# Kernel optimization log

Measured on AMD Instinct MI355X. Metric: run time of the kernel, lower is better.

The kernel has to match this reference:

```python
import jax, jax.numpy as jnp
import numpy as np

KERNEL_SIZE = 11
SIGMA = 1.5
DATA_RANGE = 1.0
C1 = (0.01 * DATA_RANGE) ** 2
C2 = (0.03 * DATA_RANGE) ** 2


def _gaussian_kernel_2d(kernel_size=KERNEL_SIZE, sigma=SIGMA):
    coords = jnp.arange(kernel_size, dtype=jnp.float32) - kernel_size // 2
    g1d = jnp.exp(-coords ** 2 / (2.0 * sigma ** 2))
    g2d = g1d[:, None] * g1d[None, :]
    return g2d / g2d.sum()  # [K, K]


def _depthwise_blur(x, kernel2d):
    # x: [B, C, H, W]; kernel2d: [K, K] -> depthwise conv, SAME padding
    C = x.shape[1]
    k = jnp.broadcast_to(kernel2d[None, None], (C, 1, KERNEL_SIZE, KERNEL_SIZE)).astype(x.dtype)
    pad = KERNEL_SIZE // 2
    return jax.lax.conv_general_dilated(
        x, k,
        window_strides=(1, 1),
        padding=((pad, pad), (pad, pad)),
        dimension_numbers=('NCHW', 'OIHW', 'NCHW'),
        feature_group_count=C,
    )


def reference(pred, target):
    kernel2d = _gaussian_kernel_2d()
    mu_p = _depthwise_blur(pred, kernel2d)
    mu_t = _depthwise_blur(target, kernel2d)
    mu_p_sq = mu_p * mu_p
    mu_t_sq = mu_t * mu_t
    mu_pt = mu_p * mu_t
    sigma_p_sq = _depthwise_blur(pred * pred, kernel2d) - mu_p_sq
    sigma_t_sq = _depthwise_blur(target * target, kernel2d) - mu_t_sq
    sigma_pt = _depthwise_blur(pred * target, kernel2d) - mu_pt
    sigma_p_sq = jnp.clip(sigma_p_sq, 0.0, None)
    sigma_t_sq = jnp.clip(sigma_t_sq, 0.0, None)
    numerator = (2.0 * mu_pt + C1) * (2.0 * sigma_pt + C2)
    denominator = (mu_p_sq + mu_t_sq + C1) * (sigma_p_sq + sigma_t_sq + C2)
    ssim_map = numerator / denominator
    return 1.0 - jnp.mean(ssim_map)


def setup_inputs() -> dict:
    key = jax.random.key(0)
    k1, k2 = jax.random.split(key)
    shape = (16, 3, 512, 512)
    pred = jax.random.uniform(k1, shape, dtype=jnp.float32)
    target = jax.random.uniform(k2, shape, dtype=jnp.float32)
    return {"pred": pred, "target": target}
```

## Files before the change

kernel.cpp:

```cpp
#include <hip/hip_runtime.h>
#include <hip/hip_fp16.h>


#define WIDTH  512
#define HEIGHT 512
#define TW 64
#define SH 128
#define RING 48
#define RST 56
#define TILES_X 8
#define TILES_Y (HEIGHT / SH)
#define PLANES 48
#define NBLK (TILES_X * TILES_Y * PLANES)
#define NPIXF 12582912.0f

typedef _Float16 half8_t __attribute__((ext_vector_type(8)));
typedef float f32x4_t __attribute__((ext_vector_type(4)));
typedef unsigned int u32x4_t __attribute__((ext_vector_type(4)));

__device__ __forceinline__ float wsel(int i) {
    unsigned a = (unsigned)i;
    float r = 0.f;
    if (a == 5u)              r = 0.26601168f;
    if (a == 4u || a == 6u)   r = 0.21300566f;
    if (a == 3u || a == 7u)   r = 0.10936069f;
    if (a == 2u || a == 8u)   r = 0.03600077f;
    if (a == 1u || a == 9u)   r = 0.00759881f;
    if (a == 0u || a == 10u)  r = 0.00102839f;
    return r;
}

__global__ __launch_bounds__(256, 4)
void ssim_main(const float* __restrict__ pred,
               const float* __restrict__ tgt,
               float* __restrict__ partial) {
    __shared__ __align__(16) __half s_ring[4][TW][RST];
    __shared__ __align__(16) __half s_pl[4][16][80];
    __shared__ float s_red[4];

    const int tid  = threadIdx.x;
    const int wv   = tid >> 6;
    const int lane = tid & 63;
    const int r15  = lane & 15;
    const int g4   = lane >> 4;
    const int x0 = blockIdx.x * TW;
    const int y0 = blockIdx.y * SH;
    const size_t plane_off = (size_t)blockIdx.z * (WIDTH * HEIGHT);
    const float* P = pred + plane_off;
    const float* T = tgt + plane_off;
    const bool x_int = (x0 >= 8) && (x0 + TW + 8 <= WIDTH);

    const float s1 = 2.f * ((float)(_Float16)0.00102839f + (float)(_Float16)0.00759881f
                   + (float)(_Float16)0.03600077f + (float)(_Float16)0.10936069f
                   + (float)(_Float16)0.21300566f) + (float)(_Float16)0.26601168f;
    const float a   = s1 * s1;
    const float C1A = a * a * 1e-4f;
    const float C2A = a * a * 9e-4f;

    half8_t Bh, Bv;
#pragma unroll
    for (int jj = 0; jj < 8; ++jj) {
        int k = g4 * 8 + jj;
        Bv[jj] = (_Float16)wsel(k - r15);
        Bh[jj] = (_Float16)wsel(k - r15 - 3);
    }

    const int  erow0 = tid >> 4, ecq0 = tid & 15;
    const bool e2    = tid < 64;
    const int  erow1 = tid >> 2, ecq1 = 16 + (tid & 3);

    auto ldquad = [&](int gybase, int row, int cq, float4& p, float4& t) {
        int gy = gybase + row;
        if (gy < 0) gy = 0;
        if (gy > HEIGHT - 1) gy = HEIGHT - 1;
        int gx = x0 - 8 + cq * 4;
        if (gx < 0) gx = 0;
        if (gx > WIDTH - 4) gx = WIDTH - 4;
        const size_t ro = (size_t)gy << 9;
        p = *(const float4*)(P + ro + gx);
        t = *(const float4*)(T + ro + gx);
    };
    auto load_gen = [&](int gybase, float4& p0, float4& t0,
                        float4& p1, float4& t1) {
        ldquad(gybase, erow0, ecq0, p0, t0);
        if (e2) ldquad(gybase, erow1, ecq1, p1, t1);
    };

    auto equad = [&](int gybase, int row, int cq, float4 pv, float4 tv) {
        int gy = gybase + row;
        if ((unsigned)gy >= (unsigned)HEIGHT) {
            pv.x = pv.y = pv.z = pv.w = 0.f;
            tv.x = tv.y = tv.z = tv.w = 0.f;
        } else if (!x_int) {
            int gx0 = x0 - 8 + cq * 4;
            if ((unsigned)(gx0 + 0) >= (unsigned)WIDTH) { pv.x = 0.f; tv.x = 0.f; }
            if ((unsigned)(gx0 + 1) >= (unsigned)WIDTH) { pv.y = 0.f; tv.y = 0.f; }
            if ((unsigned)(gx0 + 2) >= (unsigned)WIDTH) { pv.z = 0.f; tv.z = 0.f; }
            if ((unsigned)(gx0 + 3) >= (unsigned)WIDTH) { pv.w = 0.f; tv.w = 0.f; }
        }
        float u0 = fmaf(pv.x, pv.x, tv.x * tv.x), v0 = pv.x * tv.x;
        float u1 = fmaf(pv.y, pv.y, tv.y * tv.y), v1 = pv.y * tv.y;
        float u2 = fmaf(pv.z, pv.z, tv.z * tv.z), v2 = pv.z * tv.z;
        float u3 = fmaf(pv.w, pv.w, tv.w * tv.w), v3 = pv.w * tv.w;
        uint2 wp, wt, wu, wvv;
        wp.x  = __builtin_bit_cast(unsigned, __floats2half2_rn(pv.x, pv.y));
        wp.y  = __builtin_bit_cast(unsigned, __floats2half2_rn(pv.z, pv.w));
        wt.x  = __builtin_bit_cast(unsigned, __floats2half2_rn(tv.x, tv.y));
        wt.y  = __builtin_bit_cast(unsigned, __floats2half2_rn(tv.z, tv.w));
        wu.x  = __builtin_bit_cast(unsigned, __floats2half2_rn(u0, u1));
        wu.y  = __builtin_bit_cast(unsigned, __floats2half2_rn(u2, u3));
        wvv.x = __builtin_bit_cast(unsigned, __floats2half2_rn(v0, v1));
        wvv.y = __builtin_bit_cast(unsigned, __floats2half2_rn(v2, v3));
        *(uint2*)&s_pl[0][row][cq * 4] = wp;
        *(uint2*)&s_pl[1][row][cq * 4] = wt;
        *(uint2*)&s_pl[2][row][cq * 4] = wu;
        *(uint2*)&s_pl[3][row][cq * 4] = wvv;
    };
    auto ewise = [&](int gybase, float4 p0, float4 t0, float4 p1, float4 t1) {
        equad(gybase, erow0, ecq0, p0, t0);
        if (e2) equad(gybase, erow1, ecq1, p1, t1);
    };

    auto hblur = [&](int relbase) {
        int s0 = relbase + 4 * g4;
        if (s0 >= 96) s0 -= 96; else if (s0 >= 48) s0 -= 48;
        const int colA = (wv << 4) + r15;
        const int acol = (wv << 4) + (g4 << 3);
#pragma unroll
        for (int q = 0; q < 4; ++q) {
            u32x4_t ra = *(const u32x4_t*)&s_pl[q][r15][acol];
            f32x4_t z = {0.f, 0.f, 0.f, 0.f};
            f32x4_t d = __builtin_amdgcn_mfma_f32_16x16x32_f16(
                __builtin_bit_cast(half8_t, ra), Bh, z, 0, 0, 0);
            uint2 pk;
            pk.x = __builtin_bit_cast(unsigned, __floats2half2_rn(d[0], d[1]));
            pk.y = __builtin_bit_cast(unsigned, __floats2half2_rn(d[2], d[3]));
            *(uint2*)&s_ring[q][colA][s0] = pk;
        }
    };

    float lsum = 0.f;

    auto vblur = [&](int jstep) {
        int sg = 16 * jstep + (g4 << 3);
        if (sg >= 96) sg -= 96; else if (sg >= 48) sg -= 48;
        const int colA = (wv << 4) + r15;
        f32x4_t acc[4];
#pragma unroll
        for (int q = 0; q < 4; ++q) {
            u32x4_t ra = *(const u32x4_t*)&s_ring[q][colA][sg];
            f32x4_t z = {0.f, 0.f, 0.f, 0.f};
            acc[q] = __builtin_amdgcn_mfma_f32_16x16x32_f16(
                __builtin_bit_cast(half8_t, ra), Bv, z, 0, 0, 0);
        }
#pragma unroll
        for (int r = 0; r < 4; ++r) {
            float mp = acc[0][r], mt = acc[1][r];
            float U  = acc[2][r], V  = acc[3][r];
            float mpt  = mp * mt;
            float B2   = fmaf(mp, mp, mt * mt);
            float S    = fmaf(a, V, -mpt);
            float Ssum = fmaf(a, U, -B2);
            float num = fmaf(2.f, mpt, C1A) * fmaf(2.f, S, C2A);
            float den = (B2 + C1A) * (Ssum + C2A);
            lsum += __fdividef(num, den);
        }
    };

    float4 ap0, at0, ap1, at1;
    float4 bp0, bt0, bp1, bt1;
    load_gen(y0 - 5, ap0, at0, ap1, at1);
    load_gen(y0 + 7, bp0, bt0, bp1, bt1);
    {
        u32x4_t z4 = {0u, 0u, 0u, 0u};
#pragma unroll
        for (int i = 0; i < 7; ++i)
            ((u32x4_t*)s_ring)[tid + 256 * i] = z4;
    }
    ewise(y0 - 5, ap0, at0, ap1, at1);
    __syncthreads();
    hblur(0);
    load_gen(y0 + 23, ap0, at0, ap1, at1);
    __syncthreads();
    ewise(y0 + 7, bp0, bt0, bp1, bt1);
    __syncthreads();
    hblur(12);
    __syncthreads();

#pragma unroll 1
    for (int j = 0; j < 8; ++j) {
        if (j < 7) ewise(y0 + 16 * j + 23, ap0, at0, ap1, at1);
        __syncthreads();
        if (j < 6) load_gen(y0 + 16 * (j + 1) + 23, ap0, at0, ap1, at1);
        if (j < 7) hblur(16 * j + 28);
        vblur(j);
        __syncthreads();
    }

#pragma unroll
    for (int off = 32; off > 0; off >>= 1) lsum += __shfl_down(lsum, off);
    if ((tid & 63) == 0) s_red[tid >> 6] = lsum;
    __syncthreads();
    if (tid == 0) {
        partial[(blockIdx.z * TILES_Y + blockIdx.y) * TILES_X + blockIdx.x] =
            s_red[0] + s_red[1] + s_red[2] + s_red[3];
    }
}

__global__ __launch_bounds__(256)
void ssim_final(const float* __restrict__ partial, float* __restrict__ out) {
    __shared__ float s_red[4];
    float s = 0.f;
    for (int i = threadIdx.x; i < NBLK; i += 256) s += partial[i];
#pragma unroll
    for (int off = 32; off > 0; off >>= 1) s += __shfl_down(s, off);
    if ((threadIdx.x & 63) == 0) s_red[threadIdx.x >> 6] = s;
    __syncthreads();
    if (threadIdx.x == 0) {
        float total = s_red[0] + s_red[1] + s_red[2] + s_red[3];
        out[0] = 1.0f - total / NPIXF;
    }
}

extern "C" void kernel_launch(void* const* d_in, const int* in_sizes, int n_in,
                              void* d_out, int out_size, void* d_ws, size_t ws_size,
                              hipStream_t stream) {
    const float* pred = (const float*)d_in[0];
    const float* tgt  = (const float*)d_in[1];
    float* partial = (float*)d_ws;

    dim3 grid(TILES_X, TILES_Y, PLANES);
    ssim_main<<<grid, dim3(256), 0, stream>>>(pred, tgt, partial);
    ssim_final<<<1, dim3(256), 0, stream>>>(partial, (float*)d_out);
}
```

Measured before the change: 130.6 us.

## Build horizontal-blur MFMA fragments directly from global loads, drop staging LDS

```diff
diff --git a/kernel.cpp b/kernel.cpp
--- a/kernel.cpp
+++ b/kernel.cpp
@@ -30,12 +30,15 @@
     return r;
 }
 
+__device__ __forceinline__ unsigned cvt2(float a, float b) {
+    return __builtin_bit_cast(unsigned, __floats2half2_rn(a, b));
+}
+
 __global__ __launch_bounds__(256, 4)
 void ssim_main(const float* __restrict__ pred,
                const float* __restrict__ tgt,
                float* __restrict__ partial) {
     __shared__ __align__(16) __half s_ring[4][TW][RST];
-    __shared__ __align__(16) __half s_pl[4][16][80];
     __shared__ float s_red[4];
 
     const int tid  = threadIdx.x;
@@ -48,7 +51,9 @@
     const size_t plane_off = (size_t)blockIdx.z * (WIDTH * HEIGHT);
     const float* P = pred + plane_off;
     const float* T = tgt + plane_off;
-    const bool x_int = (x0 >= 8) && (x0 + TW + 8 <= WIDTH);
+
+    const int gxb  = x0 - 8 + (wv << 4) + (g4 << 3);
+    const int colA = (wv << 4) + r15;
 
     const float s1 = 2.f * ((float)(_Float16)0.00102839f + (float)(_Float16)0.00759881f
                    + (float)(_Float16)0.03600077f + (float)(_Float16)0.10936069f
@@ -65,78 +70,67 @@
         Bh[jj] = (_Float16)wsel(k - r15 - 3);
     }
 
-    const int  erow0 = tid >> 4, ecq0 = tid & 15;
-    const bool e2    = tid < 64;
-    const int  erow1 = tid >> 2, ecq1 = 16 + (tid & 3);
-
-    auto ldquad = [&](int gybase, int row, int cq, float4& p, float4& t) {
-        int gy = gybase + row;
+    auto load8 = [&](int gybase, float4& p0, float4& p1,
+                     float4& t0, float4& t1) {
+        int gy = gybase + r15;
         if (gy < 0) gy = 0;
         if (gy > HEIGHT - 1) gy = HEIGHT - 1;
-        int gx = x0 - 8 + cq * 4;
-        if (gx < 0) gx = 0;
-        if (gx > WIDTH - 4) gx = WIDTH - 4;
-        const size_t ro = (size_t)gy << 9;
-        p = *(const float4*)(P + ro + gx);
-        t = *(const float4*)(T + ro + gx);
-    };
-    auto load_gen = [&](int gybase, float4& p0, float4& t0,
-                        float4& p1, float4& t1) {
-        ldquad(gybase, erow0, ecq0, p0, t0);
-        if (e2) ldquad(gybase, erow1, ecq1, p1, t1);
-    };
-
-    auto equad = [&](int gybase, int row, int cq, float4 pv, float4 tv) {
-        int gy = gybase + row;
-        if ((unsigned)gy >= (unsigned)HEIGHT) {
-            pv.x = pv.y = pv.z = pv.w = 0.f;
-            tv.x = tv.y = tv.z = tv.w = 0.f;
-        } else if (!x_int) {
-            int gx0 = x0 - 8 + cq * 4;
-            if ((unsigned)(gx0 + 0) >= (unsigned)WIDTH) { pv.x = 0.f; tv.x = 0.f; }
-            if ((unsigned)(gx0 + 1) >= (unsigned)WIDTH) { pv.y = 0.f; tv.y = 0.f; }
-            if ((unsigned)(gx0 + 2) >= (unsigned)WIDTH) { pv.z = 0.f; tv.z = 0.f; }
-            if ((unsigned)(gx0 + 3) >= (unsigned)WIDTH) { pv.w = 0.f; tv.w = 0.f; }
-        }
-        float u0 = fmaf(pv.x, pv.x, tv.x * tv.x), v0 = pv.x * tv.x;
-        float u1 = fmaf(pv.y, pv.y, tv.y * tv.y), v1 = pv.y * tv.y;
-        float u2 = fmaf(pv.z, pv.z, tv.z * tv.z), v2 = pv.z * tv.z;
-        float u3 = fmaf(pv.w, pv.w, tv.w * tv.w), v3 = pv.w * tv.w;
-        uint2 wp, wt, wu, wvv;
-        wp.x  = __builtin_bit_cast(unsigned, __floats2half2_rn(pv.x, pv.y));
-        wp.y  = __builtin_bit_cast(unsigned, __floats2half2_rn(pv.z, pv.w));
-        wt.x  = __builtin_bit_cast(unsigned, __floats2half2_rn(tv.x, tv.y));
-        wt.y  = __builtin_bit_cast(unsigned, __floats2half2_rn(tv.z, tv.w));
-        wu.x  = __builtin_bit_cast(unsigned, __floats2half2_rn(u0, u1));
-        wu.y  = __builtin_bit_cast(unsigned, __floats2half2_rn(u2, u3));
-        wvv.x = __builtin_bit_cast(unsigned, __floats2half2_rn(v0, v1));
-        wvv.y = __builtin_bit_cast(unsigned, __floats2half2_rn(v2, v3));
-        *(uint2*)&s_pl[0][row][cq * 4] = wp;
-        *(uint2*)&s_pl[1][row][cq * 4] = wt;
-        *(uint2*)&s_pl[2][row][cq * 4] = wu;
-        *(uint2*)&s_pl[3][row][cq * 4] = wvv;
-    };
-    auto ewise = [&](int gybase, float4 p0, float4 t0, float4 p1, float4 t1) {
-        equad(gybase, erow0, ecq0, p0, t0);
-        if (e2) equad(gybase, erow1, ecq1, p1, t1);
-    };
-
-    auto hblur = [&](int relbase) {
+        int gxc = gxb;
+        if (gxc < 0) gxc = 0;
+        if (gxc > WIDTH - 8) gxc = WIDTH - 8;
+        const float* pr = P + ((size_t)gy << 9) + gxc;
+        const float* tr = T + ((size_t)gy << 9) + gxc;
+        p0 = *(const float4*)pr; p1 = *(const float4*)(pr + 4);
+        t0 = *(const float4*)tr; t1 = *(const float4*)(tr + 4);
+    };
+
+    auto make_frags = [&](int gybase, float4 pv0, float4 pv1,
+                          float4 tv0, float4 tv1, u32x4_t* F) {
+        int gy = gybase + r15;
+        const bool ok = ((unsigned)gy < (unsigned)HEIGHT) &&
+                        ((unsigned)gxb <= (unsigned)(WIDTH - 8));
+        if (!ok) {
+            pv0.x = pv0.y = pv0.z = pv0.w = 0.f;
+            pv1.x = pv1.y = pv1.z = pv1.w = 0.f;
+            tv0.x = tv0.y = tv0.z = tv0.w = 0.f;
+            tv1.x = tv1.y = tv1.z = tv1.w = 0.f;
+        }
+        float u0 = fmaf(pv0.x, pv0.x, tv0.x * tv0.x), v0 = pv0.x * tv0.x;
+        float u1 = fmaf(pv0.y, pv0.y, tv0.y * tv0.y), v1 = pv0.y * tv0.y;
+        float u2 = fmaf(pv0.z, pv0.z, tv0.z * tv0.z), v2 = pv0.z * tv0.z;
+        float u3 = fmaf(pv0.w, pv0.w, tv0.w * tv0.w), v3 = pv0.w * tv0.w;
+        float u4 = fmaf(pv1.x, pv1.x, tv1.x * tv1.x), v4 = pv1.x * tv1.x;
+        float u5 = fmaf(pv1.y, pv1.y, tv1.y * tv1.y), v5 = pv1.y * tv1.y;
+        float u6 = fmaf(pv1.z, pv1.z, tv1.z * tv1.z), v6 = pv1.z * tv1.z;
+        float u7 = fmaf(pv1.w, pv1.w, tv1.w * tv1.w), v7 = pv1.w * tv1.w;
+        u32x4_t Pu, Tu, Uu, Vu;
+        Pu[0] = cvt2(pv0.x, pv0.y); Pu[1] = cvt2(pv0.z, pv0.w);
+        Pu[2] = cvt2(pv1.x, pv1.y); Pu[3] = cvt2(pv1.z, pv1.w);
+        Tu[0] = cvt2(tv0.x, tv0.y); Tu[1] = cvt2(tv0.z, tv0.w);
+        Tu[2] = cvt2(tv1.x, tv1.y); Tu[3] = cvt2(tv1.z, tv1.w);
+        Uu[0] = cvt2(u0, u1); Uu[1] = cvt2(u2, u3);
+        Uu[2] = cvt2(u4, u5); Uu[3] = cvt2(u6, u7);
+        Vu[0] = cvt2(v0, v1); Vu[1] = cvt2(v2, v3);
+        Vu[2] = cvt2(v4, v5); Vu[3] = cvt2(v6, v7);
+        F[0] = Pu; F[1] = Tu; F[2] = Uu; F[3] = Vu;
+    };
+
+    auto hcompute = [&](const u32x4_t* F, uint2* dpk) {
+#pragma unroll
+        for (int q = 0; q < 4; ++q) {
+            f32x4_t z = {0.f, 0.f, 0.f, 0.f};
+            f32x4_t d = __builtin_amdgcn_mfma_f32_16x16x32_f16(
+                __builtin_bit_cast(half8_t, F[q]), Bh, z, 0, 0, 0);
+            dpk[q].x = cvt2(d[0], d[1]);
+            dpk[q].y = cvt2(d[2], d[3]);
+        }
+    };
+    auto hstore = [&](const uint2* dpk, int relbase) {
         int s0 = relbase + 4 * g4;
         if (s0 >= 96) s0 -= 96; else if (s0 >= 48) s0 -= 48;
-        const int colA = (wv << 4) + r15;
-        const int acol = (wv << 4) + (g4 << 3);
-#pragma unroll
-        for (int q = 0; q < 4; ++q) {
-            u32x4_t ra = *(const u32x4_t*)&s_pl[q][r15][acol];
-            f32x4_t z = {0.f, 0.f, 0.f, 0.f};
-            f32x4_t d = __builtin_amdgcn_mfma_f32_16x16x32_f16(
-                __builtin_bit_cast(half8_t, ra), Bh, z, 0, 0, 0);
-            uint2 pk;
-            pk.x = __builtin_bit_cast(unsigned, __floats2half2_rn(d[0], d[1]));
-            pk.y = __builtin_bit_cast(unsigned, __floats2half2_rn(d[2], d[3]));
-            *(uint2*)&s_ring[q][colA][s0] = pk;
-        }
+#pragma unroll
+        for (int q = 0; q < 4; ++q)
+            *(uint2*)&s_ring[q][colA][s0] = dpk[q];
     };
 
     float lsum = 0.f;
@@ -144,7 +138,6 @@
     auto vblur = [&](int jstep) {
         int sg = 16 * jstep + (g4 << 3);
         if (sg >= 96) sg -= 96; else if (sg >= 48) sg -= 48;
-        const int colA = (wv << 4) + r15;
         f32x4_t acc[4];
 #pragma unroll
         for (int q = 0; q < 4; ++q) {
@@ -167,33 +160,41 @@
         }
     };
 
-    float4 ap0, at0, ap1, at1;
-    float4 bp0, bt0, bp1, bt1;
-    load_gen(y0 - 5, ap0, at0, ap1, at1);
-    load_gen(y0 + 7, bp0, bt0, bp1, bt1);
+    float4 rp0, rp1, rt0, rt1;
+    float4 sp0, sp1, st0, st1;
+    load8(y0 - 5, rp0, rp1, rt0, rt1);
+    load8(y0 + 7, sp0, sp1, st0, st1);
     {
         u32x4_t z4 = {0u, 0u, 0u, 0u};
 #pragma unroll
         for (int i = 0; i < 7; ++i)
             ((u32x4_t*)s_ring)[tid + 256 * i] = z4;
     }
-    ewise(y0 - 5, ap0, at0, ap1, at1);
-    __syncthreads();
-    hblur(0);
-    load_gen(y0 + 23, ap0, at0, ap1, at1);
-    __syncthreads();
-    ewise(y0 + 7, bp0, bt0, bp1, bt1);
-    __syncthreads();
-    hblur(12);
+    u32x4_t F2[4], F1[4];
+    uint2 d2[4], d1[4];
+    make_frags(y0 - 5, rp0, rp1, rt0, rt1, F2);
+    hcompute(F2, d2);
+    make_frags(y0 + 7, sp0, sp1, st0, st1, F1);
+    hcompute(F1, d1);
+    load8(y0 + 23, rp0, rp1, rt0, rt1);
+    __syncthreads();
+    hstore(d2, 0);
+    __syncthreads();
+    hstore(d1, 12);
     __syncthreads();
 
 #pragma unroll 1
     for (int j = 0; j < 8; ++j) {
-        if (j < 7) ewise(y0 + 16 * j + 23, ap0, at0, ap1, at1);
+        u32x4_t F[4];
+        uint2 dpk[4];
+        if (j < 7) {
+            make_frags(y0 + 16 * j + 23, rp0, rp1, rt0, rt1, F);
+            hcompute(F, dpk);
+        }
+        vblur(j);
         __syncthreads();
-        if (j < 6) load_gen(y0 + 16 * (j + 1) + 23, ap0, at0, ap1, at1);
-        if (j < 7) hblur(16 * j + 28);
-        vblur(j);
+        if (j < 7) hstore(dpk, 16 * j + 28);
+        if (j < 6) load8(y0 + 16 * (j + 1) + 23, rp0, rp1, rt0, rt1);
         __syncthreads();
     }
 
```

After: 137.2 us. +5.0%, slower.

## Double-buffer global prefetch and reblock ring LDS layout to avoid bank conflicts

Applied to the files above, without the earlier changes.

```diff
diff --git a/kernel.cpp b/kernel.cpp
--- a/kernel.cpp
+++ b/kernel.cpp
@@ -7,7 +7,6 @@
 #define TW 64
 #define SH 128
 #define RING 48
-#define RST 56
 #define TILES_X 8
 #define TILES_Y (HEIGHT / SH)
 #define PLANES 48
@@ -30,12 +29,16 @@
     return r;
 }
 
+__device__ __forceinline__ unsigned cvt2(float a, float b) {
+    return __builtin_bit_cast(unsigned, __floats2half2_rn(a, b));
+}
+
 __global__ __launch_bounds__(256, 4)
 void ssim_main(const float* __restrict__ pred,
                const float* __restrict__ tgt,
                float* __restrict__ partial) {
-    __shared__ __align__(16) __half s_ring[4][TW][RST];
-    __shared__ __align__(16) __half s_pl[4][16][80];
+    __shared__ __align__(16) __half s_ring[4][RING / 8][TW][8];
+    __shared__ __align__(16) __half s_pl[4][16][88];
     __shared__ float s_red[4];
 
     const int tid  = threadIdx.x;
@@ -50,6 +53,8 @@
     const float* T = tgt + plane_off;
     const bool x_int = (x0 >= 8) && (x0 + TW + 8 <= WIDTH);
 
+    const int colA = (wv << 4) + r15;
+
     const float s1 = 2.f * ((float)(_Float16)0.00102839f + (float)(_Float16)0.00759881f
                    + (float)(_Float16)0.03600077f + (float)(_Float16)0.10936069f
                    + (float)(_Float16)0.21300566f) + (float)(_Float16)0.26601168f;
@@ -103,14 +108,10 @@
         float u2 = fmaf(pv.z, pv.z, tv.z * tv.z), v2 = pv.z * tv.z;
         float u3 = fmaf(pv.w, pv.w, tv.w * tv.w), v3 = pv.w * tv.w;
         uint2 wp, wt, wu, wvv;
-        wp.x  = __builtin_bit_cast(unsigned, __floats2half2_rn(pv.x, pv.y));
-        wp.y  = __builtin_bit_cast(unsigned, __floats2half2_rn(pv.z, pv.w));
-        wt.x  = __builtin_bit_cast(unsigned, __floats2half2_rn(tv.x, tv.y));
-        wt.y  = __builtin_bit_cast(unsigned, __floats2half2_rn(tv.z, tv.w));
-        wu.x  = __builtin_bit_cast(unsigned, __floats2half2_rn(u0, u1));
-        wu.y  = __builtin_bit_cast(unsigned, __floats2half2_rn(u2, u3));
-        wvv.x = __builtin_bit_cast(unsigned, __floats2half2_rn(v0, v1));
-        wvv.y = __builtin_bit_cast(unsigned, __floats2half2_rn(v2, v3));
+        wp.x  = cvt2(pv.x, pv.y); wp.y  = cvt2(pv.z, pv.w);
+        wt.x  = cvt2(tv.x, tv.y); wt.y  = cvt2(tv.z, tv.w);
+        wu.x  = cvt2(u0, u1);     wu.y  = cvt2(u2, u3);
+        wvv.x = cvt2(v0, v1);     wvv.y = cvt2(v2, v3);
         *(uint2*)&s_pl[0][row][cq * 4] = wp;
         *(uint2*)&s_pl[1][row][cq * 4] = wt;
         *(uint2*)&s_pl[2][row][cq * 4] = wu;
@@ -124,7 +125,7 @@
     auto hblur = [&](int relbase) {
         int s0 = relbase + 4 * g4;
         if (s0 >= 96) s0 -= 96; else if (s0 >= 48) s0 -= 48;
-        const int colA = (wv << 4) + r15;
+        const int sb = s0 >> 3, si = s0 & 7;
         const int acol = (wv << 4) + (g4 << 3);
 #pragma unroll
         for (int q = 0; q < 4; ++q) {
@@ -133,9 +134,9 @@
             f32x4_t d = __builtin_amdgcn_mfma_f32_16x16x32_f16(
                 __builtin_bit_cast(half8_t, ra), Bh, z, 0, 0, 0);
             uint2 pk;
-            pk.x = __builtin_bit_cast(unsigned, __floats2half2_rn(d[0], d[1]));
-            pk.y = __builtin_bit_cast(unsigned, __floats2half2_rn(d[2], d[3]));
-            *(uint2*)&s_ring[q][colA][s0] = pk;
+            pk.x = cvt2(d[0], d[1]);
+            pk.y = cvt2(d[2], d[3]);
+            *(uint2*)&s_ring[q][sb][colA][si] = pk;
         }
     };
 
@@ -144,11 +145,11 @@
     auto vblur = [&](int jstep) {
         int sg = 16 * jstep + (g4 << 3);
         if (sg >= 96) sg -= 96; else if (sg >= 48) sg -= 48;
-        const int colA = (wv << 4) + r15;
+        const int sb = sg >> 3;
         f32x4_t acc[4];
 #pragma unroll
         for (int q = 0; q < 4; ++q) {
-            u32x4_t ra = *(const u32x4_t*)&s_ring[q][colA][sg];
+            u32x4_t ra = *(const u32x4_t*)&s_ring[q][sb][colA][0];
             f32x4_t z = {0.f, 0.f, 0.f, 0.f};
             acc[q] = __builtin_amdgcn_mfma_f32_16x16x32_f16(
                 __builtin_bit_cast(half8_t, ra), Bv, z, 0, 0, 0);
@@ -167,31 +168,38 @@
         }
     };
 
-    float4 ap0, at0, ap1, at1;
-    float4 bp0, bt0, bp1, bt1;
-    load_gen(y0 - 5, ap0, at0, ap1, at1);
-    load_gen(y0 + 7, bp0, bt0, bp1, bt1);
+    float4 Ap0, At0, Ap1, At1;
+    float4 Bp0, Bt0, Bp1, Bt1;
+    load_gen(y0 - 5, Ap0, At0, Ap1, At1);
+    load_gen(y0 + 7, Bp0, Bt0, Bp1, Bt1);
     {
         u32x4_t z4 = {0u, 0u, 0u, 0u};
 #pragma unroll
-        for (int i = 0; i < 7; ++i)
-            ((u32x4_t*)s_ring)[tid + 256 * i] = z4;
-    }
-    ewise(y0 - 5, ap0, at0, ap1, at1);
+        for (int i = 0; i < RING / 8; ++i)
+            *(u32x4_t*)&s_ring[g4][i][colA][0] = z4;
+    }
+    ewise(y0 - 5, Ap0, At0, Ap1, At1);
     __syncthreads();
     hblur(0);
-    load_gen(y0 + 23, ap0, at0, ap1, at1);
-    __syncthreads();
-    ewise(y0 + 7, bp0, bt0, bp1, bt1);
+    load_gen(y0 + 23, Ap0, At0, Ap1, At1);
+    __syncthreads();
+    ewise(y0 + 7, Bp0, Bt0, Bp1, Bt1);
     __syncthreads();
     hblur(12);
+    load_gen(y0 + 39, Bp0, Bt0, Bp1, Bt1);
     __syncthreads();
 
 #pragma unroll 1
     for (int j = 0; j < 8; ++j) {
-        if (j < 7) ewise(y0 + 16 * j + 23, ap0, at0, ap1, at1);
+        if (j < 7) {
+            if (j & 1) ewise(y0 + 16 * j + 23, Bp0, Bt0, Bp1, Bt1);
+            else       ewise(y0 + 16 * j + 23, Ap0, At0, Ap1, At1);
+        }
         __syncthreads();
-        if (j < 6) load_gen(y0 + 16 * (j + 1) + 23, ap0, at0, ap1, at1);
+        if (j < 5) {
+            if (j & 1) load_gen(y0 + 16 * (j + 2) + 23, Bp0, Bt0, Bp1, Bt1);
+            else       load_gen(y0 + 16 * (j + 2) + 23, Ap0, At0, Ap1, At1);
+        }
         if (j < 7) hblur(16 * j + 28);
         vblur(j);
         __syncthreads();
```

After: 133.5 us. 2.2% more time.
